# Kernel optimization log

Measured on AMD Instinct MI355X. Metric: run time of the kernel, lower is better.

## Reference

```python
import jax, jax.numpy as jnp
from jax import lax
import numpy as np

KERNEL = 32
ORISIZE = 256
EPS = 1e-5


def _avgpool(x, k):
    # x: [B, C, H, W] -> [B, C, H-k+1, W-k+1], stride 1, VALID
    s = lax.reduce_window(x, 0.0, lax.add, (1, 1, k, k), (1, 1, 1, 1), 'VALID')
    return s / float(k * k)


def setup_inputs() -> dict:
    key = jax.random.key(0)
    k1, k2, k3, k4 = jax.random.split(key, 4)
    B, C = 32, 64
    return {
        'infeat': jax.random.normal(k1, (B, 2, ORISIZE, ORISIZE), jnp.float32),
        'labelTpesudo': jax.random.uniform(k2, (B, 1, ORISIZE, ORISIZE), jnp.float32),
        'labelT': jax.random.uniform(k3, (B, 1, ORISIZE, ORISIZE), jnp.float32),
        'FeatureDA': jax.random.normal(k4, (B, C, ORISIZE, ORISIZE), jnp.float32),
        'k': 2,
    }


def reference(infeat, labelTpesudo, labelT, FeatureDA, k):
    B = infeat.shape[0]
    P = ORISIZE - KERNEL + 1  # poolSize = 225
    half = KERNEL // 2        # suppression half-window = 16

    prob = jax.nn.softmax(infeat, axis=1)                      # F.softmax default dim=1 for 4D
    ent = -prob * jnp.log(prob + EPS)                          # Entropy()
    entP = jnp.sum(_avgpool(ent, KERNEL), axis=1)              # [B, P, P]
    featP = _avgpool(prob, KERNEL)                             # [B, 2, P, P]

    def extract(src, py, px):  # src [C,H,W] -> [C,KERNEL,KERNEL]
        return lax.dynamic_slice(src, (0, py, px), (src.shape[0], KERNEL, KERNEL))
    extract_b = jax.vmap(extract, in_axes=(0, 0, 0))

    grid = jnp.arange(P)
    cls_list, feat_list, lp_list, lt_list, val_list, oxy_list = [], [], [], [], [], []

    for c in range(2):  # class loop (unchg, chg)
        mask = jnp.ones((B, P, P), infeat.dtype)
        for _kk in range(k):  # greedy top-k with suppression
            filt = (featP[:, c] - 0.1 * entP) * mask           # [B, P, P]
            flat = filt.reshape(B, -1)
            idx = jnp.argmax(flat, axis=1)                     # topk k=1
            vals = jnp.take_along_axis(flat, idx[:, None], axis=1)[:, 0]
            py = idx // P
            px = idx % P
            # suppression box in pooled coords (half-open, clipped to [0, P])
            y0 = jnp.maximum(0, py - half); y1 = jnp.minimum(P, py + half)
            x0 = jnp.maximum(0, px - half); x1 = jnp.minimum(P, px + half)
            box = ((grid[None, :, None] >= y0[:, None, None]) & (grid[None, :, None] < y1[:, None, None]) &
                   (grid[None, None, :] >= x0[:, None, None]) & (grid[None, None, :] < x1[:, None, None]))
            mask = mask * (1.0 - box.astype(mask.dtype))
            # patch extraction in image coords: py,px <= P-1 so 32x32 always fits
            cls_list.append(extract_b(infeat, py, px))
            feat_list.append(extract_b(FeatureDA, py, px))
            lp_list.append(extract_b(labelTpesudo, py, px))
            lt_list.append(extract_b(labelT, py, px))
            val_list.append(vals)
            ox = jnp.stack([px, px + KERNEL - 1], axis=1)
            oy = jnp.stack([py, py + KERNEL - 1], axis=1)
            oxy_list.append(jnp.stack([ox, oy], axis=1).astype(jnp.int32))  # [B,2,2]

    classiferT = jnp.concatenate(cls_list, axis=0)   # [2*k*B, 2, 32, 32]
    patchFeatDA = jnp.concatenate(feat_list, axis=0)  # [2*k*B, C, 32, 32]
    labelpesudo = jnp.concatenate(lp_list, axis=0)
    labelTTrue = jnp.concatenate(lt_list, axis=0)
    provalue = jnp.concatenate(val_list, axis=0)      # [2*k*B]
    pointXY = jnp.concatenate(oxy_list, axis=0)       # [2*k*B, 2, 2]
    return classiferT, patchFeatDA, labelpesudo, labelTTrue, provalue, pointXY
```

## Files before the change

### kernel.cpp

```cpp
#include <hip/hip_runtime.h>
#include <math.h>

#define ORISIZE 256
#define KER 32
#define P 225
#define PP (P * P)
#define HALF 16
#define FEPS 1e-5f
#define NSPLIT 32
#define CHUNK ((PP + NSPLIT - 1) / NSPLIT)

__global__ __launch_bounds__(256) void field_hpool_kernel(
    const float* __restrict__ infeat, float* __restrict__ Hp,
    float* __restrict__ He) {
  int b = blockIdx.x >> 8;
  int y = blockIdx.x & 255;
  int x = threadIdx.x;

  __shared__ float sp[ORISIZE];
  __shared__ float se[ORISIZE];

  const float* r0 = infeat + ((size_t)(b * 2 + 0) * ORISIZE + y) * ORISIZE;
  const float* r1 = infeat + ((size_t)(b * 2 + 1) * ORISIZE + y) * ORISIZE;
  float a0 = r0[x];
  float a1 = r1[x];
  float m = fmaxf(a0, a1);
  float e0 = expf(a0 - m);
  float e1 = expf(a1 - m);
  float s = e0 + e1;
  float p0 = e0 / s;
  float p1 = e1 / s;
  float ent = -(p0 * logf(p0 + FEPS)) - (p1 * logf(p1 + FEPS));
  sp[x] = p0;
  se[x] = ent;
  __syncthreads();

  if (x < P) {
    float accp = 0.f, acce = 0.f;
#pragma unroll
    for (int dx = 0; dx < KER; ++dx) {
      accp += sp[x + dx];
      acce += se[x + dx];
    }
    size_t o = ((size_t)b * ORISIZE + y) * P + x;
    Hp[o] = accp;
    He[o] = acce;
  }
}

__global__ __launch_bounds__(256) void vpool_kernel(
    const float* __restrict__ Hp, const float* __restrict__ He,
    float* __restrict__ F, int B, int total) {
  int idx = blockIdx.x * blockDim.x + threadIdx.x;
  if (idx >= total) return;
  int b = idx / PP;
  int r = idx - b * PP;
  int py = r / P;
  int px = r - py * P;
  const float* hp = Hp + ((size_t)b * ORISIZE + py) * P + px;
  const float* he = He + ((size_t)b * ORISIZE + py) * P + px;
  float a = 0.f, e = 0.f;
#pragma unroll
  for (int dy = 0; dy < KER; ++dy) {
    a += hp[(size_t)dy * P];
    e += he[(size_t)dy * P];
  }
  float sv = a * (1.f / (KER * KER));
  float ev = e * (1.f / (KER * KER));
  F[(size_t)(0 * B + b) * PP + r] = sv - 0.1f * ev;
  F[(size_t)(1 * B + b) * PP + r] = (1.0f - sv) - 0.1f * ev;
}

__global__ __launch_bounds__(256) void argmax_round_kernel(
    const float* __restrict__ F, float* __restrict__ pval,
    int* __restrict__ pidx, int B, int kk) {
  int s = blockIdx.x;
  int b = blockIdx.y;
  int c = blockIdx.z;
  int tid = threadIdx.x;

  __shared__ int bys[16], bxs[16];
  __shared__ float rv[256];
  __shared__ int ri[256];

  if (tid < kk) {
    int j = tid;
    int pbase = ((j * B + b) * 2 + c) * NSPLIT;
    float bv = -INFINITY;
    int bi = PP;
    for (int ss = 0; ss < NSPLIT; ++ss) {
      float v = pval[pbase + ss];
      int ii = pidx[pbase + ss];
      if (v > bv || (v == bv && ii < bi)) { bv = v; bi = ii; }
    }
    int py = bi / P;
    bys[j] = py;
    bxs[j] = bi - py * P;
  }
  __syncthreads();

  const float* f = F + ((size_t)c * B + b) * PP;
  int base = s * CHUNK;
  int end = base + CHUNK;
  if (end > PP) end = PP;

  float best = -INFINITY;
  int bi = PP;
  for (int i = base + tid; i < end; i += 256) {
    float v = f[i];
    int py = i / P;
    int px = i - py * P;
    bool masked = false;
    for (int j = 0; j < kk; ++j) {
      if (py >= bys[j] - HALF && py < bys[j] + HALF && px >= bxs[j] - HALF &&
          px < bxs[j] + HALF)
        masked = true;
    }
    if (masked) v = 0.0f;
    if (v > best) {
      best = v;
      bi = i;
    }
  }
  rv[tid] = best;
  ri[tid] = bi;
  __syncthreads();
  for (int sh = 128; sh > 0; sh >>= 1) {
    if (tid < sh) {
      float v2 = rv[tid + sh];
      int i2 = ri[tid + sh];
      if (v2 > rv[tid] || (v2 == rv[tid] && i2 < ri[tid])) {
        rv[tid] = v2;
        ri[tid] = i2;
      }
    }
    __syncthreads();
  }
  if (tid == 0) {
    int p = ((kk * B + b) * 2 + c) * NSPLIT + s;
    pval[p] = rv[0];
    pidx[p] = ri[0];
  }
}

__global__ __launch_bounds__(256) void finish_kernel(
    const float* __restrict__ pval, const int* __restrict__ pidx, int B, int K,
    float* __restrict__ out_val, float* __restrict__ out_xy,
    int* __restrict__ selyx) {
  int total = B * 2 * K;
  for (int t = blockIdx.x * blockDim.x + threadIdx.x; t < total;
       t += gridDim.x * blockDim.x) {
    int c = t & 1;
    int rem = t >> 1;
    int b = rem % B;
    int kk = rem / B;
    int pbase = ((kk * B + b) * 2 + c) * NSPLIT;
    float bv = -INFINITY;
    int bi = PP;
    for (int ss = 0; ss < NSPLIT; ++ss) {
      float v = pval[pbase + ss];
      int ii = pidx[pbase + ss];
      if (v > bv || (v == bv && ii < bi)) { bv = v; bi = ii; }
    }
    int py = bi / P;
    int px = bi - py * P;
    int slot = (c * K + kk) * B + b;
    out_val[slot] = bv;
    out_xy[slot * 4 + 0] = (float)px;
    out_xy[slot * 4 + 1] = (float)(px + KER - 1);
    out_xy[slot * 4 + 2] = (float)py;
    out_xy[slot * 4 + 3] = (float)(py + KER - 1);
    selyx[slot * 2 + 0] = py;
    selyx[slot * 2 + 1] = px;
  }
}

__global__ __launch_bounds__(256) void extract_all_kernel(
    const float* __restrict__ infeat, const float* __restrict__ FeatureDA,
    const float* __restrict__ lp, const float* __restrict__ lt,
    const int* __restrict__ selyx, int B, int C, int total,
    float* __restrict__ out, size_t o_feat, size_t o_lp, size_t o_lt) {
  int idx = blockIdx.x * blockDim.x + threadIdx.x;
  if (idx >= total) return;
  int TC = C + 4;
  int per = TC * KER * KER;
  int slot = idx / per;
  int rem = idx - slot * per;
  int tc = rem >> 10;
  int pix = rem & 1023;
  int dy = pix >> 5;
  int dx = pix & 31;
  int b = slot % B;
  int py = selyx[slot * 2 + 0];
  int px = selyx[slot * 2 + 1];

  const float* src;
  int ch, srcC;
  size_t dsto;
  if (tc < 2) {
    src = infeat; ch = tc; srcC = 2;
    dsto = ((size_t)slot * 2 + ch) * 1024;
  } else if (tc < 2 + C) {
    src = FeatureDA; ch = tc - 2; srcC = C;
    dsto = o_feat + ((size_t)slot * C + ch) * 1024;
  } else if (tc == 2 + C) {
    src = lp; ch = 0; srcC = 1;
    dsto = o_lp + (size_t)slot * 1024;
  } else {
    src = lt; ch = 0; srcC = 1;
    dsto = o_lt + (size_t)slot * 1024;
  }
  out[dsto + pix] =
      src[(((size_t)b * srcC + ch) * ORISIZE + (py + dy)) * ORISIZE + (px + dx)];
}

extern "C" void kernel_launch(void* const* d_in, const int* in_sizes, int n_in,
                              void* d_out, int out_size, void* d_ws,
                              size_t ws_size, hipStream_t stream) {
  const float* infeat = (const float*)d_in[0];
  const float* labelTpesudo = (const float*)d_in[1];
  const float* labelT = (const float*)d_in[2];
  const float* FeatureDA = (const float*)d_in[3];

  int B = in_sizes[0] / (2 * ORISIZE * ORISIZE);
  int C = in_sizes[3] / (B * ORISIZE * ORISIZE);
  long per_patch = (long)(C + 4) * KER * KER + 5;
  int K = (int)((long)out_size / (2L * B * per_patch));
  if (K < 1) K = 1;
  if (K > 16) K = 16;
  int npatch = 2 * K * B;

  float* Hp = (float*)d_ws;
  float* He = Hp + (size_t)B * ORISIZE * P;
  float* F = He + (size_t)B * ORISIZE * P;
  float* pval = F + (size_t)2 * B * PP;
  int* pidx = (int*)(pval + (size_t)16 * B * 2 * NSPLIT);
  int* selyx = pidx + (size_t)16 * B * 2 * NSPLIT;

  float* out = (float*)d_out;
  size_t o_feat = (size_t)npatch * 2 * KER * KER;
  size_t o_lp = o_feat + (size_t)npatch * C * KER * KER;
  size_t o_lt = o_lp + (size_t)npatch * KER * KER;
  size_t o_val = o_lt + (size_t)npatch * KER * KER;
  size_t o_xy = o_val + (size_t)npatch;

  field_hpool_kernel<<<dim3(B * ORISIZE), dim3(256), 0, stream>>>(infeat, Hp,
                                                                  He);

  int totalv = B * PP;
  vpool_kernel<<<dim3((totalv + 255) / 256), dim3(256), 0, stream>>>(
      Hp, He, F, B, totalv);

  for (int kk = 0; kk < K; ++kk) {
    argmax_round_kernel<<<dim3(NSPLIT, B, 2), dim3(256), 0, stream>>>(
        F, pval, pidx, B, kk);
  }
  finish_kernel<<<dim3(1), dim3(256), 0, stream>>>(pval, pidx, B, K,
                                                   out + o_val, out + o_xy,
                                                   selyx);

  int total = npatch * (C + 4) * KER * KER;
  extract_all_kernel<<<dim3((total + 255) / 256), dim3(256), 0, stream>>>(
      infeat, FeatureDA, labelTpesudo, labelT, selyx, B, C, total, out, o_feat,
      o_lp, o_lt);
}
```

Baseline: 707.5 us.

## Fuse horizontal and vertical pooling with shared ring buffer; vectorize patch extraction

```diff
diff --git a/kernel.cpp b/kernel.cpp
--- a/kernel.cpp
+++ b/kernel.cpp
@@ -9,66 +9,88 @@
 #define FEPS 1e-5f
 #define NSPLIT 32
 #define CHUNK ((PP + NSPLIT - 1) / NSPLIT)
-
-__global__ __launch_bounds__(256) void field_hpool_kernel(
-    const float* __restrict__ infeat, float* __restrict__ Hp,
-    float* __restrict__ He) {
-  int b = blockIdx.x >> 8;
-  int y = blockIdx.x & 255;
-  int x = threadIdx.x;
-
-  __shared__ float sp[ORISIZE];
-  __shared__ float se[ORISIZE];
-
-  const float* r0 = infeat + ((size_t)(b * 2 + 0) * ORISIZE + y) * ORISIZE;
-  const float* r1 = infeat + ((size_t)(b * 2 + 1) * ORISIZE + y) * ORISIZE;
-  float a0 = r0[x];
-  float a1 = r1[x];
-  float m = fmaxf(a0, a1);
-  float e0 = expf(a0 - m);
-  float e1 = expf(a1 - m);
-  float s = e0 + e1;
-  float p0 = e0 / s;
-  float p1 = e1 / s;
-  float ent = -(p0 * logf(p0 + FEPS)) - (p1 * logf(p1 + FEPS));
-  sp[x] = p0;
-  se[x] = ent;
-  __syncthreads();
-
-  if (x < P) {
-    float accp = 0.f, acce = 0.f;
+#define TILE_W 32
+#define NTILE 8
+#define RCH 8
+#define RING 40
+
+__global__ __launch_bounds__(256) void pool_kernel(
+    const float* __restrict__ infeat, float* __restrict__ F, int B) {
+  int tile = blockIdx.x;
+  int b = blockIdx.y;
+  int tid = threadIdx.x;
+  int px0 = tile * TILE_W;
+  int tw = P - px0;
+  if (tw > TILE_W) tw = TILE_W;
+  int iw = tw + KER - 1;
+
+  __shared__ float s_p[RCH][64];
+  __shared__ float s_e[RCH][64];
+  __shared__ float ring_p[RING][TILE_W];
+  __shared__ float ring_e[RING][TILE_W];
+
+  const float* in0 = infeat + (size_t)(b * 2 + 0) * ORISIZE * ORISIZE + px0;
+  const float* in1 = infeat + (size_t)(b * 2 + 1) * ORISIZE * ORISIZE + px0;
+
+  for (int c0 = 0; c0 < ORISIZE; c0 += RCH) {
+    for (int it = tid; it < RCH * 64; it += 256) {
+      int r = it >> 6;
+      int xi = it & 63;
+      if (xi < iw) {
+        int y = c0 + r;
+        float a0 = in0[(size_t)y * ORISIZE + xi];
+        float a1 = in1[(size_t)y * ORISIZE + xi];
+        float m = fmaxf(a0, a1);
+        float e0 = expf(a0 - m);
+        float e1 = expf(a1 - m);
+        float s = e0 + e1;
+        float p0 = e0 / s;
+        float p1 = e1 / s;
+        float ent = -(p0 * logf(p0 + FEPS)) - (p1 * logf(p1 + FEPS));
+        s_p[r][xi] = p0;
+        s_e[r][xi] = ent;
+      }
+    }
+    __syncthreads();
+
+    {
+      int r = tid >> 5;
+      int px = tid & 31;
+      if (px < tw) {
+        float accp = 0.f, acce = 0.f;
 #pragma unroll
-    for (int dx = 0; dx < KER; ++dx) {
-      accp += sp[x + dx];
-      acce += se[x + dx];
-    }
-    size_t o = ((size_t)b * ORISIZE + y) * P + x;
-    Hp[o] = accp;
-    He[o] = acce;
-  }
-}
-
-__global__ __launch_bounds__(256) void vpool_kernel(
-    const float* __restrict__ Hp, const float* __restrict__ He,
-    float* __restrict__ F, int B, int total) {
-  int idx = blockIdx.x * blockDim.x + threadIdx.x;
-  if (idx >= total) return;
-  int b = idx / PP;
-  int r = idx - b * PP;
-  int py = r / P;
-  int px = r - py * P;
-  const float* hp = Hp + ((size_t)b * ORISIZE + py) * P + px;
-  const float* he = He + ((size_t)b * ORISIZE + py) * P + px;
-  float a = 0.f, e = 0.f;
+        for (int dx = 0; dx < KER; ++dx) {
+          accp += s_p[r][px + dx];
+          acce += s_e[r][px + dx];
+        }
+        int slot = (c0 + r) % RING;
+        ring_p[slot][px] = accp;
+        ring_e[slot][px] = acce;
+      }
+    }
+    __syncthreads();
+
+    {
+      int pyi = tid >> 5;
+      int px = tid & 31;
+      int py = c0 - (KER - 1) + pyi;
+      if (py >= 0 && py < P && px < tw) {
+        float a = 0.f, e = 0.f;
+        int slot = py % RING;
 #pragma unroll
-  for (int dy = 0; dy < KER; ++dy) {
-    a += hp[(size_t)dy * P];
-    e += he[(size_t)dy * P];
-  }
-  float sv = a * (1.f / (KER * KER));
-  float ev = e * (1.f / (KER * KER));
-  F[(size_t)(0 * B + b) * PP + r] = sv - 0.1f * ev;
-  F[(size_t)(1 * B + b) * PP + r] = (1.0f - sv) - 0.1f * ev;
+        for (int dy = 0; dy < KER; ++dy) {
+          a += ring_p[slot][px];
+          e += ring_e[slot][px];
+          if (++slot == RING) slot = 0;
+        }
+        float sv = a * (1.f / (KER * KER));
+        float ev = e * (1.f / (KER * KER));
+        size_t o = (size_t)b * PP + (size_t)py * P + px0 + px;
+        F[o] = sv - 0.1f * ev;
+        F[(size_t)B * PP + o] = (1.0f - sv) - 0.1f * ev;
+      }
+    }
+  }
 }
 
 __global__ __launch_bounds__(256) void argmax_round_kernel(
@@ -175,21 +197,15 @@
   }
 }
 
-__global__ __launch_bounds__(256) void extract_all_kernel(
+__global__ __launch_bounds__(256) void extract_kernel(
     const float* __restrict__ infeat, const float* __restrict__ FeatureDA,
     const float* __restrict__ lp, const float* __restrict__ lt,
-    const int* __restrict__ selyx, int B, int C, int total,
-    float* __restrict__ out, size_t o_feat, size_t o_lp, size_t o_lt) {
-  int idx = blockIdx.x * blockDim.x + threadIdx.x;
-  if (idx >= total) return;
+    const int* __restrict__ selyx, int B, int C, float* __restrict__ out,
+    size_t o_feat, size_t o_lp, size_t o_lt) {
   int TC = C + 4;
-  int per = TC * KER * KER;
-  int slot = idx / per;
-  int rem = idx - slot * per;
-  int tc = rem >> 10;
-  int pix = rem & 1023;
-  int dy = pix >> 5;
-  int dx = pix & 31;
+  int plane = blockIdx.x;
+  int slot = plane / TC;
+  int tc = plane - slot * TC;
   int b = slot % B;
   int py = selyx[slot * 2 + 0];
   int px = selyx[slot * 2 + 1];
@@ -210,8 +226,18 @@
     src = lt; ch = 0; srcC = 1;
     dsto = o_lt + (size_t)slot * 1024;
   }
-  out[dsto + pix] =
-      src[(((size_t)b * srcC + ch) * ORISIZE + (py + dy)) * ORISIZE + (px + dx)];
+
+  int pix = threadIdx.x * 4;
+  int dy = pix >> 5;
+  int dx = pix & 31;
+  const float* srow =
+      src + (((size_t)b * srcC + ch) * ORISIZE + (py + dy)) * ORISIZE + px + dx;
+  float4 v;
+  v.x = srow[0];
+  v.y = srow[1];
+  v.z = srow[2];
+  v.w = srow[3];
+  *reinterpret_cast<float4*>(out + dsto + pix) = v;
 }
 
 extern "C" void kernel_launch(void* const* d_in, const int* in_sizes, int n_in,
@@ -230,9 +256,7 @@
   if (K > 16) K = 16;
   int npatch = 2 * K * B;
 
-  float* Hp = (float*)d_ws;
-  float* He = Hp + (size_t)B * ORISIZE * P;
-  float* F = He + (size_t)B * ORISIZE * P;
+  float* F = (float*)d_ws;
   float* pval = F + (size_t)2 * B * PP;
   int* pidx = (int*)(pval + (size_t)16 * B * 2 * NSPLIT);
   int* selyx = pidx + (size_t)16 * B * 2 * NSPLIT;
@@ -244,12 +268,7 @@
   size_t o_val = o_lt + (size_t)npatch * KER * KER;
   size_t o_xy = o_val + (size_t)npatch;
 
-  field_hpool_kernel<<<dim3(B * ORISIZE), dim3(256), 0, stream>>>(infeat, Hp,
-                                                                  He);
-
-  int totalv = B * PP;
-  vpool_kernel<<<dim3((totalv + 255) / 256), dim3(256), 0, stream>>>(
-      Hp, He, F, B, totalv);
+  pool_kernel<<<dim3(NTILE, B), dim3(256), 0, stream>>>(infeat, F, B);
 
   for (int kk = 0; kk < K; ++kk) {
     argmax_round_kernel<<<dim3(NSPLIT, B, 2), dim3(256), 0, stream>>>(
@@ -259,8 +278,8 @@
                                                    out + o_val, out + o_xy,
                                                    selyx);
 
-  int total = npatch * (C + 4) * KER * KER;
-  extract_all_kernel<<<dim3((total + 255) / 256), dim3(256), 0, stream>>>(
-      infeat, FeatureDA, labelTpesudo, labelT, selyx, B, C, total, out, o_feat,
-      o_lp, o_lt);
-}
+  int nplanes = npatch * (C + 4);
+  extract_kernel<<<dim3(nplanes), dim3(256), 0, stream>>>(
+      infeat, FeatureDA, labelTpesudo, labelT, selyx, B, C, out, o_feat, o_lp,
+      o_lt);
+}
```

Result: no change. 718.6 us (+1.6%).
